# Kernel tuning notes

Hardware: AMD Instinct MI355X
Metric: run time of the kernel (lower is better)

Reference implementation:

```python
import jax, jax.numpy as jnp
import numpy as np

# Fuzzy-logic decoder: rules = [[0,0,0],[1,0,1]] (hardcoded in the torch module's __init__).
# For each rule [p, a, b] firing on predicate p:
#   num[s,o] = max_k min(t[a, s, k], t[b, k, o])   (max-min relation composition)
# amalgamate(x, y) = x + y - x*y (probabilistic OR); new starts at 0, and
# amalgamate(x, 0) = x, so with exactly one rule per predicate:
#   t_new[p] = amalgamate(t[p], num_p) = t[p] + num_p - t[p]*num_p

def _compose(A, B):
    # A: [S, K], B: [K, O] -> max over k of elementwise min -> [S, O]
    return jnp.max(jnp.minimum(A[:, :, None], B[None, :, :]), axis=1)


def setup_inputs() -> dict:
    key = jax.random.key(0)
    t = jax.random.uniform(key, (2, 512, 512), dtype=jnp.float32)
    return {"t": t}


def reference(t) -> jnp.ndarray:
    t0, t1 = t[0], t[1]
    num0 = _compose(t0, t0)          # rule [0,0,0]
    num1 = _compose(t0, t1)          # rule [1,0,1]
    num = jnp.stack([num0, num1], axis=0)  # [2, S, O]
    return t + num - t * num         # amalgamate(t, num)
```

## Files before the change

### kernel.cpp

```cpp
#include <hip/hip_runtime.h>


#define SDIM 512
#define TS 64
#define TO 32
#define BK 64
#define BK2 32
#define NCH (SDIM / BK)
#define ASTR 36

typedef _Float16 h2 __attribute__((ext_vector_type(2)));

__device__ __forceinline__ h2 pack2(float a, float b) {
    return __builtin_bit_cast(h2, __builtin_amdgcn_cvt_pkrtz(a, b));
}
__device__ __forceinline__ h2 pmin(h2 a, h2 b) { return __builtin_elementwise_min(a, b); }
__device__ __forceinline__ h2 pmax(h2 a, h2 b) { return __builtin_elementwise_max(a, b); }

__global__ __launch_bounds__(256) void fuzzy_compose_kernel(
        const float* __restrict__ t, float* __restrict__ out) {
    __shared__ h2 Als[TS][ASTR];
    __shared__ h2 Bls[BK2][TO];

    const int tid = threadIdx.x;
    const int o0 = blockIdx.x * TO;
    const int s0 = blockIdx.y * TS;
    const int p  = blockIdx.z;

    const float* __restrict__ A = t;
    const float* __restrict__ B = t + p * (SDIM * SDIM);

    const int og = tid & 15, sg = tid >> 4;
    const int ol = og * 2, sl = sg * 4;

    const int ar = tid >> 2, aq = tid & 3;
    const int bk = tid >> 3, bq = tid & 7;

    const float4* __restrict__ Arow =
        reinterpret_cast<const float4*>(A + (s0 + ar) * SDIM);

    h2 acc[4][2];
    #pragma unroll
    for (int j = 0; j < 4; ++j)
        #pragma unroll
        for (int i = 0; i < 2; ++i)
            acc[j][i] = pack2(0.f, 0.f);

    float4 fa[4], fx, fy;
    #pragma unroll
    for (int q4 = 0; q4 < 4; ++q4) fa[q4] = Arow[aq * 4 + q4];
    fx = *reinterpret_cast<const float4*>(B + (2 * bk) * SDIM + o0 + bq * 4);
    fy = *reinterpret_cast<const float4*>(B + (2 * bk + 1) * SDIM + o0 + bq * 4);

    for (int c = 0; c < NCH; ++c) {
        #pragma unroll
        for (int q4 = 0; q4 < 4; ++q4) {
            Als[ar][aq * 8 + q4 * 2 + 0] = pack2(fa[q4].x, fa[q4].y);
            Als[ar][aq * 8 + q4 * 2 + 1] = pack2(fa[q4].z, fa[q4].w);
        }
        Bls[bk][bq * 4 + 0] = pack2(fx.x, fy.x);
        Bls[bk][bq * 4 + 1] = pack2(fx.y, fy.y);
        Bls[bk][bq * 4 + 2] = pack2(fx.z, fy.z);
        Bls[bk][bq * 4 + 3] = pack2(fx.w, fy.w);
        __syncthreads();

        if (c + 1 < NCH) {
            const int k0 = (c + 1) * BK;
            #pragma unroll
            for (int q4 = 0; q4 < 4; ++q4) fa[q4] = Arow[k0 / 4 + aq * 4 + q4];
            fx = *reinterpret_cast<const float4*>(B + (k0 + 2 * bk) * SDIM + o0 + bq * 4);
            fy = *reinterpret_cast<const float4*>(B + (k0 + 2 * bk + 1) * SDIM + o0 + bq * 4);
        }

        #pragma unroll
        for (int k2 = 0; k2 < BK2; ++k2) {
            const h2 b0 = Bls[k2][ol];
            const h2 b1 = Bls[k2][ol + 1];
            #pragma unroll
            for (int j = 0; j < 4; ++j) {
                const h2 a = Als[sl + j][k2];
                acc[j][0] = pmax(acc[j][0], pmin(a, b0));
                acc[j][1] = pmax(acc[j][1], pmin(a, b1));
            }
        }
        __syncthreads();
    }

    const float* __restrict__ tp = t + p * (SDIM * SDIM);
    float* __restrict__ op = out + p * (SDIM * SDIM);
    #pragma unroll
    for (int j = 0; j < 4; ++j) {
        const int row = s0 + sl + j;
        const float2 tv = *reinterpret_cast<const float2*>(tp + row * SDIM + o0 + ol);
        const float n0 = fmaxf((float)acc[j][0][0], (float)acc[j][0][1]);
        const float n1 = fmaxf((float)acc[j][1][0], (float)acc[j][1][1]);
        float2 r;
        r.x = tv.x + n0 - tv.x * n0;
        r.y = tv.y + n1 - tv.y * n1;
        *reinterpret_cast<float2*>(op + row * SDIM + o0 + ol) = r;
    }
}

extern "C" void kernel_launch(void* const* d_in, const int* in_sizes, int n_in,
                              void* d_out, int out_size, void* d_ws, size_t ws_size,
                              hipStream_t stream) {
    const float* t = (const float*)d_in[0];
    float* out = (float*)d_out;
    dim3 grid(SDIM / TO, SDIM / TS, 2);
    fuzzy_compose_kernel<<<grid, 256, 0, stream>>>(t, out);
}
```

Before: 72.22 us.

## Shrink row tile to 2x2 per thread with k-quad packed LDS layout

Halves the row tile to 32, doubling the block count, and gives each thread a 2x2 output micro-tile. Both A and B are stored in LDS as k-major uint2 entries, each holding four consecutive k values as packed half pairs. The inner loop issues two 128-bit LDS reads per k-quad in place of many 32-bit reads. The global prefetch moves ahead of the barrier, the last barrier is dropped, and the launch bound requests two blocks per CU. The aim is more parallelism and fewer LDS instructions, at the cost of lower arithmetic reuse per LDS byte (2x2 versus 4x2 per thread).

```diff
diff --git a/kernel.cpp b/kernel.cpp
--- a/kernel.cpp
+++ b/kernel.cpp
@@ -2,12 +2,12 @@
 
 
 #define SDIM 512
-#define TS 64
+#define TS 32
 #define TO 32
-#define BK 64
-#define BK2 32
-#define NCH (SDIM / BK)
-#define ASTR 36
+#define BK 128
+#define NKQ 32
+#define NCH 4
+#define RSTR 34
 
 typedef _Float16 h2 __attribute__((ext_vector_type(2)));
 
@@ -16,84 +16,107 @@
 }
 __device__ __forceinline__ h2 pmin(h2 a, h2 b) { return __builtin_elementwise_min(a, b); }
 __device__ __forceinline__ h2 pmax(h2 a, h2 b) { return __builtin_elementwise_max(a, b); }
+__device__ __forceinline__ h2 bch2(unsigned u) { return __builtin_bit_cast(h2, u); }
+__device__ __forceinline__ unsigned b32(h2 v) { return __builtin_bit_cast(unsigned, v); }
 
-__global__ __launch_bounds__(256) void fuzzy_compose_kernel(
+__global__ __launch_bounds__(256, 2) void fuzzy_compose_kernel(
         const float* __restrict__ t, float* __restrict__ out) {
-    __shared__ h2 Als[TS][ASTR];
-    __shared__ h2 Bls[BK2][TO];
+    __shared__ uint2 A2[NKQ][RSTR];
+    __shared__ uint2 B2[NKQ][RSTR];
 
     const int tid = threadIdx.x;
     const int o0 = blockIdx.x * TO;
     const int s0 = blockIdx.y * TS;
     const int p  = blockIdx.z;
+    const float* __restrict__ Bmat = t + p * (SDIM * SDIM);
 
-    const float* __restrict__ A = t;
-    const float* __restrict__ B = t + p * (SDIM * SDIM);
+    const int ol = (tid & 15) * 2;
+    const int sl = (tid >> 4) * 2;
 
-    const int og = tid & 15, sg = tid >> 4;
-    const int ol = og * 2, sl = sg * 4;
-
-    const int ar = tid >> 2, aq = tid & 3;
-    const int bk = tid >> 3, bq = tid & 7;
+    const int ar = tid >> 3, aq = tid & 7;
+    const int bkq = tid >> 3, bq = tid & 7;
 
     const float4* __restrict__ Arow =
-        reinterpret_cast<const float4*>(A + (s0 + ar) * SDIM);
+        reinterpret_cast<const float4*>(t + (s0 + ar) * SDIM);
 
-    h2 acc[4][2];
+    h2 acc[2][2][2];
     #pragma unroll
-    for (int j = 0; j < 4; ++j)
+    for (int j = 0; j < 2; ++j)
         #pragma unroll
-        for (int i = 0; i < 2; ++i)
-            acc[j][i] = pack2(0.f, 0.f);
+        for (int i = 0; i < 2; ++i) {
+            acc[j][i][0] = pack2(0.f, 0.f);
+            acc[j][i][1] = pack2(0.f, 0.f);
+        }
 
-    float4 fa[4], fx, fy;
+    float4 fa[4], fb[4];
     #pragma unroll
-    for (int q4 = 0; q4 < 4; ++q4) fa[q4] = Arow[aq * 4 + q4];
-    fx = *reinterpret_cast<const float4*>(B + (2 * bk) * SDIM + o0 + bq * 4);
-    fy = *reinterpret_cast<const float4*>(B + (2 * bk + 1) * SDIM + o0 + bq * 4);
+    for (int q = 0; q < 4; ++q) fa[q] = Arow[aq + 8 * q];
+    #pragma unroll
+    for (int r = 0; r < 4; ++r)
+        fb[r] = *reinterpret_cast<const float4*>(Bmat + (4 * bkq + r) * SDIM + o0 + bq * 4);
 
     for (int c = 0; c < NCH; ++c) {
         #pragma unroll
-        for (int q4 = 0; q4 < 4; ++q4) {
-            Als[ar][aq * 8 + q4 * 2 + 0] = pack2(fa[q4].x, fa[q4].y);
-            Als[ar][aq * 8 + q4 * 2 + 1] = pack2(fa[q4].z, fa[q4].w);
+        for (int q = 0; q < 4; ++q) {
+            const int f = aq + 8 * q;
+            uint2 u;
+            u.x = b32(pack2(fa[q].x, fa[q].y));
+            u.y = b32(pack2(fa[q].z, fa[q].w));
+            A2[f][ar] = u;
         }
-        Bls[bk][bq * 4 + 0] = pack2(fx.x, fy.x);
-        Bls[bk][bq * 4 + 1] = pack2(fx.y, fy.y);
-        Bls[bk][bq * 4 + 2] = pack2(fx.z, fy.z);
-        Bls[bk][bq * 4 + 3] = pack2(fx.w, fy.w);
+        {
+            uint4 u01, u23;
+            u01.x = b32(pack2(fb[0].x, fb[1].x)); u01.y = b32(pack2(fb[2].x, fb[3].x));
+            u01.z = b32(pack2(fb[0].y, fb[1].y)); u01.w = b32(pack2(fb[2].y, fb[3].y));
+            u23.x = b32(pack2(fb[0].z, fb[1].z)); u23.y = b32(pack2(fb[2].z, fb[3].z));
+            u23.z = b32(pack2(fb[0].w, fb[1].w)); u23.w = b32(pack2(fb[2].w, fb[3].w));
+            *reinterpret_cast<uint4*>(&B2[bkq][bq * 4 + 0]) = u01;
+            *reinterpret_cast<uint4*>(&B2[bkq][bq * 4 + 2]) = u23;
+        }
+
+        if (c + 1 < NCH) {
+            const int kf4 = (c + 1) * (BK / 4);
+            #pragma unroll
+            for (int q = 0; q < 4; ++q) fa[q] = Arow[kf4 + aq + 8 * q];
+            #pragma unroll
+            for (int r = 0; r < 4; ++r)
+                fb[r] = *reinterpret_cast<const float4*>(
+                    Bmat + ((c + 1) * BK + 4 * bkq + r) * SDIM + o0 + bq * 4);
+        }
+
         __syncthreads();
 
-        if (c + 1 < NCH) {
-            const int k0 = (c + 1) * BK;
-            #pragma unroll
-            for (int q4 = 0; q4 < 4; ++q4) fa[q4] = Arow[k0 / 4 + aq * 4 + q4];
-            fx = *reinterpret_cast<const float4*>(B + (k0 + 2 * bk) * SDIM + o0 + bq * 4);
-            fy = *reinterpret_cast<const float4*>(B + (k0 + 2 * bk + 1) * SDIM + o0 + bq * 4);
+        #pragma unroll
+        for (int kq = 0; kq < NKQ; ++kq) {
+            const uint4 ua = *reinterpret_cast<const uint4*>(&A2[kq][sl]);
+            const uint4 ub = *reinterpret_cast<const uint4*>(&B2[kq][ol]);
+            const h2 a0e = bch2(ua.x), a0o = bch2(ua.y);
+            const h2 a1e = bch2(ua.z), a1o = bch2(ua.w);
+            const h2 b0e = bch2(ub.x), b0o = bch2(ub.y);
+            const h2 b1e = bch2(ub.z), b1o = bch2(ub.w);
+            acc[0][0][0] = pmax(acc[0][0][0], pmin(a0e, b0e));
+            acc[0][0][1] = pmax(acc[0][0][1], pmin(a0o, b0o));
+            acc[0][1][0] = pmax(acc[0][1][0], pmin(a0e, b1e));
+            acc[0][1][1] = pmax(acc[0][1][1], pmin(a0o, b1o));
+            acc[1][0][0] = pmax(acc[1][0][0], pmin(a1e, b0e));
+            acc[1][0][1] = pmax(acc[1][0][1], pmin(a1o, b0o));
+            acc[1][1][0] = pmax(acc[1][1][0], pmin(a1e, b1e));
+            acc[1][1][1] = pmax(acc[1][1][1], pmin(a1o, b1o));
         }
 
-        #pragma unroll
-        for (int k2 = 0; k2 < BK2; ++k2) {
-            const h2 b0 = Bls[k2][ol];
-            const h2 b1 = Bls[k2][ol + 1];
-            #pragma unroll
-            for (int j = 0; j < 4; ++j) {
-                const h2 a = Als[sl + j][k2];
-                acc[j][0] = pmax(acc[j][0], pmin(a, b0));
-                acc[j][1] = pmax(acc[j][1], pmin(a, b1));
-            }
-        }
-        __syncthreads();
+        if (c + 1 < NCH) __syncthreads();
     }
 
     const float* __restrict__ tp = t + p * (SDIM * SDIM);
     float* __restrict__ op = out + p * (SDIM * SDIM);
     #pragma unroll
-    for (int j = 0; j < 4; ++j) {
+    for (int j = 0; j < 2; ++j) {
         const int row = s0 + sl + j;
         const float2 tv = *reinterpret_cast<const float2*>(tp + row * SDIM + o0 + ol);
-        const float n0 = fmaxf((float)acc[j][0][0], (float)acc[j][0][1]);
-        const float n1 = fmaxf((float)acc[j][1][0], (float)acc[j][1][1]);
+        const h2 m0 = pmax(acc[j][0][0], acc[j][0][1]);
+        const h2 m1 = pmax(acc[j][1][0], acc[j][1][1]);
+        const float n0 = fmaxf((float)m0[0], (float)m0[1]);
+        const float n1 = fmaxf((float)m1[0], (float)m1[1]);
         float2 r;
         r.x = tv.x + n0 - tv.x * n0;
         r.y = tv.y + n1 - tv.y * n1;
```

Measured after the change: 95.28 us. 31.9% more time.
